# Kernel optimization log

Measured on AMD Instinct MI355X. Metric: run time of the kernel, lower is better.

## Reference

```python
import jax, jax.numpy as jnp
import numpy as np

EMBED_DIM = 1024
NUM_HEADS = 16
HEAD_DIM = EMBED_DIM // NUM_HEADS  # 64
SCALE = HEAD_DIM ** -0.5


def _rope_table(seq_len, dtype=jnp.float32):
    # inv_freq: [head_dim/2]
    inv_freq = 1.0 / (10000.0 ** (jnp.arange(0, HEAD_DIM, 2, dtype=dtype) / HEAD_DIM))
    t = jnp.arange(seq_len, dtype=dtype)
    freqs = t[:, None] * inv_freq[None, :]  # [S, hd/2]
    return jnp.sin(freqs), jnp.cos(freqs)


def _apply_rope(x, sin, cos):
    # x: [B, H, S, hd]; sin/cos: [S, hd/2]
    sin = sin[None, None]
    cos = cos[None, None]
    x_even = x[..., 0::2]
    x_odd = x[..., 1::2]
    new_even = x_even * cos - x_odd * sin
    new_odd = x_even * sin + x_odd * cos
    # interleave back: [..., hd/2, 2] -> [..., hd]
    return jnp.stack((new_even, new_odd), axis=-1).reshape(x.shape)


def setup_inputs() -> dict:
    key = jax.random.key(0)
    ks = jax.random.split(key, 9)
    B, S, D = 2, 2048, EMBED_DIM
    s = D ** -0.5
    return {
        "query": jax.random.normal(ks[0], (B, S, D), dtype=jnp.float32),
        "Wq": jax.random.normal(ks[1], (2 * D, D), dtype=jnp.float32) * s,
        "bq": jnp.zeros((2 * D,), dtype=jnp.float32),
        "Wk": jax.random.normal(ks[2], (D, D), dtype=jnp.float32) * s,
        "bk": jnp.zeros((D,), dtype=jnp.float32),
        "Wv": jax.random.normal(ks[3], (D, D), dtype=jnp.float32) * s,
        "bv": jnp.zeros((D,), dtype=jnp.float32),
        "Wo": jax.random.normal(ks[4], (D, D), dtype=jnp.float32) * s,
        "bo": jnp.zeros((D,), dtype=jnp.float32),
    }


def reference(query, Wq, bq, Wk, bk, Wv, bv, Wo, bo):
    B, S, D = query.shape
    H, hd = NUM_HEADS, HEAD_DIM

    # QKV projections (elementwise-gate variant: q_proj outputs 2*D)
    q_raw = (query @ Wq.T + bq).reshape(B, S, H, 2 * hd)
    q = q_raw[..., :hd].transpose(0, 2, 1, 3)          # [B,H,S,hd]
    gate = q_raw[..., hd:].transpose(0, 2, 1, 3)        # [B,H,S,hd]
    k = (query @ Wk.T + bk).reshape(B, S, H, hd).transpose(0, 2, 1, 3)
    v = (query @ Wv.T + bv).reshape(B, S, H, hd).transpose(0, 2, 1, 3)

    sin, cos = _rope_table(S)
    q = _apply_rope(q, sin, cos)
    k = _apply_rope(k, sin, cos)

    # scaled dot-product attention (no mask, non-causal, dropout=0)
    scores = jnp.einsum('bhqd,bhkd->bhqk', q, k) * SCALE
    probs = jax.nn.softmax(scores, axis=-1)
    attn = jnp.einsum('bhqk,bhkd->bhqd', probs, v)

    # sigmoid elementwise gate, then output projection
    attn = attn * jax.nn.sigmoid(gate)
    out = attn.transpose(0, 2, 1, 3).reshape(B, S, D)
    return out @ Wo.T + bo
```

## Files before the change

kernel.cpp:

```cpp
#include <hip/hip_runtime.h>
#include <math.h>

#define SEQ 2048
#define DIMD 1024
#define NH 16
#define HDIM 64

typedef _Float16 h8 __attribute__((ext_vector_type(8)));
typedef _Float16 h4 __attribute__((ext_vector_type(4)));
typedef __fp16 fp16x2 __attribute__((ext_vector_type(2)));
typedef float f32x4 __attribute__((ext_vector_type(4)));

typedef const __attribute__((address_space(1))) void* gas_t;
typedef __attribute__((address_space(3))) void* las_t;

__device__ __forceinline__ int SWE(int r, int c) {
  return ((r << 6) + c) ^ ((r & 7) << 3);
}

#define R0 16384
#define R1 (R0 + 1048576)
#define R2 (R1 + 524288)
#define R3 (R2 + 262144)
#define R4 (R3 + 262144)
#define R5 (R4 + 262144)

__global__ void prep_kernel(const float* __restrict__ query,
                            const float* __restrict__ Wq,
                            const float* __restrict__ Wk,
                            const float* __restrict__ Wv,
                            const float* __restrict__ Wo,
                            _Float16* __restrict__ Ah,
                            _Float16* __restrict__ Wqh,
                            _Float16* __restrict__ Wkh,
                            _Float16* __restrict__ Wvh,
                            _Float16* __restrict__ Woh,
                            float* __restrict__ sintab,
                            float* __restrict__ costab) {
  int i = blockIdx.x * 256 + threadIdx.x;
  if (i < R0) {
#pragma unroll
    for (int j = 0; j < 4; ++j) {
      int idx = i * 4 + j;
      int tp = idx >> 5;
      int fi = idx & 31;
      double inv = pow(10000.0, -(double)(2 * fi) / 64.0);
      double a = (double)tp * inv;
      sintab[idx] = (float)sin(a);
      costab[idx] = (float)cos(a);
    }
    return;
  }
  const float* src;
  _Float16* dst;
  int k;
  if (i < R1) {
    k = i - R0; src = query; dst = Ah;
  } else if (i < R2) {
    k = i - R1; src = Wq; dst = Wqh;
  } else if (i < R3) {
    k = i - R2; src = Wk; dst = Wkh;
  } else if (i < R4) {
    k = i - R3; src = Wv; dst = Wvh;
  } else if (i < R5) {
    k = i - R4; src = Wo; dst = Woh;
  } else {
    return;
  }
  float4 v = ((const float4*)src)[k];
  h4 H;
  H[0] = (_Float16)v.x;
  H[1] = (_Float16)v.y;
  H[2] = (_Float16)v.z;
  H[3] = (_Float16)v.w;
  ((h4*)dst)[k] = H;
}

__global__ __launch_bounds__(512) void qkv_kernel(
    const _Float16* __restrict__ Ah, const _Float16* __restrict__ Wqh,
    const _Float16* __restrict__ Wkh, const _Float16* __restrict__ Wvh,
    const float* __restrict__ bq, const float* __restrict__ bk,
    const float* __restrict__ bv, _Float16* __restrict__ qw,
    _Float16* __restrict__ sg, _Float16* __restrict__ kw,
    _Float16* __restrict__ vtw, const float* __restrict__ sintab,
    const float* __restrict__ costab) {
  __shared__ _Float16 Abuf[3][16384];
  __shared__ _Float16 Bbuf[3][8192];
  const int t = threadIdx.x;
  const int lane = t & 63;
  const int w = t >> 6;
  const int wm = w >> 1;
  const int wn = w & 1;
  const int fr = lane & 15;
  const int g = lane >> 4;
  const int m0 = blockIdx.y * 256;
  const int n0 = blockIdx.x * 128;
  const int region = (n0 < 2048) ? 0 : (n0 < 3072 ? 1 : 2);
  const _Float16* Wb = region == 0   ? Wqh + (size_t)n0 * DIMD
                       : region == 1 ? Wkh + (size_t)(n0 - 2048) * DIMD
                                     : Wvh + (size_t)(n0 - 3072) * DIMD;
  const float* bias = region == 0   ? bq + n0
                      : region == 1 ? bk + (n0 - 2048)
                                    : bv + (n0 - 3072);

  f32x4 acc[4][4];
#pragma unroll
  for (int i = 0; i < 4; ++i)
#pragma unroll
    for (int j = 0; j < 4; ++j) acc[i][j] = (f32x4){0.f, 0.f, 0.f, 0.f};

  const int rsub = t >> 3;
  const int csw = ((t & 7) ^ (rsub & 7)) << 3;
  const _Float16* gA = Ah + (size_t)(m0 + rsub) * DIMD + csw;
  const _Float16* gB = Wb + (size_t)rsub * DIMD + csw;

  auto stage = [&](int kt, int bi) {
#pragma unroll
    for (int i = 0; i < 4; ++i)
      __builtin_amdgcn_global_load_lds(
          (gas_t)(gA + (size_t)i * 64 * DIMD + kt * 64),
          (las_t)&Abuf[bi][i * 4096 + t * 8], 16, 0, 0);
#pragma unroll
    for (int i = 0; i < 2; ++i)
      __builtin_amdgcn_global_load_lds(
          (gas_t)(gB + (size_t)i * 64 * DIMD + kt * 64),
          (las_t)&Bbuf[bi][i * 4096 + t * 8], 16, 0, 0);
  };

  stage(0, 0);
  stage(1, 1);
  for (int kt = 0; kt < 16; ++kt) {
    const int cb = kt % 3;
    if (kt + 1 < 16) {
      asm volatile("s_waitcnt vmcnt(6)" ::: "memory");
    } else {
      asm volatile("s_waitcnt vmcnt(0)" ::: "memory");
    }
    if (kt + 2 < 16) stage(kt + 2, (kt + 2) % 3);
    __builtin_amdgcn_sched_barrier(0);
    __builtin_amdgcn_s_barrier();
    __builtin_amdgcn_sched_barrier(0);
#pragma unroll
    for (int kk = 0; kk < 2; ++kk) {
      h8 av[4], bv[4];
#pragma unroll
      for (int mi = 0; mi < 4; ++mi)
        av[mi] =
            *(const h8*)&Abuf[cb][SWE(wm * 64 + mi * 16 + fr, 8 * g + 32 * kk)];
#pragma unroll
      for (int ni = 0; ni < 4; ++ni)
        bv[ni] =
            *(const h8*)&Bbuf[cb][SWE(wn * 64 + ni * 16 + fr, 8 * g + 32 * kk)];
      __builtin_amdgcn_s_setprio(1);
#pragma unroll
      for (int mi = 0; mi < 4; ++mi)
#pragma unroll
        for (int ni = 0; ni < 4; ++ni)
          acc[mi][ni] = __builtin_amdgcn_mfma_f32_16x16x32_f16(
              av[mi], bv[ni], acc[mi][ni], 0, 0, 0);
      __builtin_amdgcn_s_setprio(0);
    }
    __builtin_amdgcn_s_barrier();
  }

#pragma unroll
  for (int mi = 0; mi < 4; ++mi)
#pragma unroll
    for (int ni = 0; ni < 4; ++ni) {
      const int cl = wn * 64 + ni * 16 + fr;
      const float bsv = bias[cl];
      if (region == 2) {
        const int vc = (n0 - 3072) + cl;
        const int h = vc >> 6, d = vc & 63;
        const int row0 = m0 + wm * 64 + mi * 16 + g * 4;
        const int b = row0 >> 11;
        const int s0 = row0 & (SEQ - 1);
        h4 vv;
#pragma unroll
        for (int r = 0; r < 4; ++r) vv[r] = (_Float16)(acc[mi][ni][r] + bsv);
        *(h4*)&vtw[((size_t)(b * NH + h) * HDIM + d) * SEQ + s0] = vv;
        continue;
      }
#pragma unroll
      for (int r = 0; r < 4; ++r) {
        const int row = m0 + wm * 64 + mi * 16 + g * 4 + r;
        float v = acc[mi][ni][r] + bsv;
        const int b = row >> 11;
        const int s = row & (SEQ - 1);
        if (region == 0) {
          const int h = n0 >> 7;
          const int d = cl & 63;
          if (wn == 0) {
            float vp = __shfl_xor(v, 1);
            const int pi = s * 32 + (d >> 1);
            float sn = sintab[pi], cs = costab[pi];
            float rv = (d & 1) ? (vp * sn + v * cs) : (v * cs - vp * sn);
            rv *= 0.125f;
            qw[((size_t)(b * NH + h) * SEQ + s) * HDIM + d] = (_Float16)rv;
          } else {
            float gv = 1.0f / (1.0f + __expf(-v));
            sg[((size_t)(b * SEQ + s)) * DIMD + h * HDIM + d] = (_Float16)gv;
          }
        } else {
          const int kc = (n0 - 2048) + cl;
          const int h = kc >> 6, d = kc & 63;
          float vp = __shfl_xor(v, 1);
          const int pi = s * 32 + (d >> 1);
          float sn = sintab[pi], cs = costab[pi];
          float rv = (d & 1) ? (vp * sn + v * cs) : (v * cs - vp * sn);
          kw[((size_t)(b * NH + h) * SEQ + s) * HDIM + d] = (_Float16)rv;
        }
      }
    }
}

__global__ __launch_bounds__(256) void ogemm_kernel(
    const _Float16* __restrict__ ag, const _Float16* __restrict__ Woh,
    const float* __restrict__ bias, float* __restrict__ out) {
  __shared__ _Float16 Abuf[8192];
  __shared__ _Float16 Bbuf[4096];
  const int t = threadIdx.x;
  const int lane = t & 63;
  const int w = t >> 6;
  const int wm = w & 1, wn = w >> 1;
  const int fr = lane & 15;
  const int g = lane >> 4;
  const int m0 = blockIdx.y * 128, n0 = blockIdx.x * 64;

  f32x4 acc[4][2];
#pragma unroll
  for (int i = 0; i < 4; ++i)
#pragma unroll
    for (int j = 0; j < 2; ++j) acc[i][j] = (f32x4){0.f, 0.f, 0.f, 0.f};

  const int rsub = t >> 3;
  const int csw = ((t & 7) ^ (rsub & 7)) << 3;
  const _Float16* gA = ag + (size_t)(m0 + rsub) * DIMD + csw;
  const _Float16* gB = Woh + (size_t)(n0 + rsub) * DIMD + csw;

  for (int kt = 0; kt < 16; ++kt) {
#pragma unroll
    for (int i = 0; i < 4; ++i)
      __builtin_amdgcn_global_load_lds(
          (gas_t)(gA + (size_t)i * 32 * DIMD + kt * 64),
          (las_t)&Abuf[i * 2048 + t * 8], 16, 0, 0);
#pragma unroll
    for (int i = 0; i < 2; ++i)
      __builtin_amdgcn_global_load_lds(
          (gas_t)(gB + (size_t)i * 32 * DIMD + kt * 64),
          (las_t)&Bbuf[i * 2048 + t * 8], 16, 0, 0);
    __syncthreads();
#pragma unroll
    for (int s = 0; s < 2; ++s) {
      h8 av[4], bv[2];
#pragma unroll
      for (int mi = 0; mi < 4; ++mi)
        av[mi] = *(const h8*)&Abuf[SWE(wm * 64 + mi * 16 + fr, 8 * g + 32 * s)];
#pragma unroll
      for (int ni = 0; ni < 2; ++ni)
        bv[ni] = *(const h8*)&Bbuf[SWE(wn * 32 + ni * 16 + fr, 8 * g + 32 * s)];
      __builtin_amdgcn_s_setprio(1);
#pragma unroll
      for (int mi = 0; mi < 4; ++mi)
#pragma unroll
        for (int ni = 0; ni < 2; ++ni)
          acc[mi][ni] = __builtin_amdgcn_mfma_f32_16x16x32_f16(
              av[mi], bv[ni], acc[mi][ni], 0, 0, 0);
      __builtin_amdgcn_s_setprio(0);
    }
    __syncthreads();
  }

#pragma unroll
  for (int mi = 0; mi < 4; ++mi)
#pragma unroll
    for (int ni = 0; ni < 2; ++ni) {
      const int col = n0 + wn * 32 + ni * 16 + fr;
      const float bsv = bias[col];
#pragma unroll
      for (int r = 0; r < 4; ++r) {
        const int row = m0 + wm * 64 + mi * 16 + g * 4 + r;
        out[(size_t)row * DIMD + col] = acc[mi][ni][r] + bsv;
      }
    }
}

__global__ __launch_bounds__(256) void flash_kernel(
    const _Float16* __restrict__ qh, const _Float16* __restrict__ kh,
    const _Float16* __restrict__ vt, const _Float16* __restrict__ sg,
    _Float16* __restrict__ ag) {
  __shared__ _Float16 K_lds[4096];
  __shared__ _Float16 Vt_lds[4096];
  const int t = threadIdx.x;
  const int lane = t & 63;
  const int w = t >> 6;
  const int fr = lane & 15;
  const int g = lane >> 4;
  const int flat = blockIdx.x;
  const int swz = (flat & 7) * 128 + (flat >> 3);
  const int bh = swz >> 5;
  const int q0 = (swz & 31) * 64;
  const size_t kvbase = (size_t)bh * (SEQ * HDIM);

  h8 qb[2];
  {
    const _Float16* qp = qh + kvbase + (size_t)(q0 + 16 * w + fr) * HDIM + 8 * g;
    qb[0] = *(const h8*)(qp);
    qb[1] = *(const h8*)(qp + 32);
  }

  f32x4 oacc[4];
  float m_i = -1e30f, l_i = 0.f;
#pragma unroll
  for (int df = 0; df < 4; ++df) oacc[df] = (f32x4){0.f, 0.f, 0.f, 0.f};

  const int srow = t >> 2;
  const int scb = (t & 3) * 16;
  const int vbase = ((scb >> 4) >> 1) * 32 + ((scb >> 4) & 1) * 4;
  const _Float16* kp = kh + kvbase;
  const _Float16* vp = vt + kvbase + (size_t)srow * SEQ;

  h8 k0v = *(const h8*)(kp + (size_t)srow * HDIM + scb);
  h8 k1v = *(const h8*)(kp + (size_t)srow * HDIM + scb + 8);
  h8 v0v = *(const h8*)(vp + scb);
  h8 v1v = *(const h8*)(vp + scb + 8);

  for (int j0 = 0; j0 < SEQ; j0 += 64) {
    __syncthreads();
    *(h8*)&K_lds[SWE(srow, scb)] = k0v;
    *(h8*)&K_lds[SWE(srow, scb + 8)] = k1v;
    {
      h4 a0 = __builtin_shufflevector(v0v, v0v, 0, 1, 2, 3);
      h4 a1 = __builtin_shufflevector(v0v, v0v, 4, 5, 6, 7);
      h4 b0 = __builtin_shufflevector(v1v, v1v, 0, 1, 2, 3);
      h4 b1 = __builtin_shufflevector(v1v, v1v, 4, 5, 6, 7);
      *(h4*)&Vt_lds[SWE(srow, vbase)] = a0;
      *(h4*)&Vt_lds[SWE(srow, vbase + 8)] = a1;
      *(h4*)&Vt_lds[SWE(srow, vbase + 16)] = b0;
      *(h4*)&Vt_lds[SWE(srow, vbase + 24)] = b1;
    }
    if (j0 + 64 < SEQ) {
      k0v = *(const h8*)(kp + (size_t)(j0 + 64 + srow) * HDIM + scb);
      k1v = *(const h8*)(kp + (size_t)(j0 + 64 + srow) * HDIM + scb + 8);
      v0v = *(const h8*)(vp + j0 + 64 + scb);
      v1v = *(const h8*)(vp + j0 + 64 + scb + 8);
    }
    __syncthreads();

    f32x4 sacc[4];
#pragma unroll
    for (int nf = 0; nf < 4; ++nf) sacc[nf] = (f32x4){0.f, 0.f, 0.f, 0.f};

    __builtin_amdgcn_s_setprio(1);
#pragma unroll
    for (int nf = 0; nf < 4; ++nf) {
      h8 ka0 = *(const h8*)&K_lds[SWE(16 * nf + fr, 8 * g)];
      h8 ka1 = *(const h8*)&K_lds[SWE(16 * nf + fr, 32 + 8 * g)];
      sacc[nf] =
          __builtin_amdgcn_mfma_f32_16x16x32_f16(ka0, qb[0], sacc[nf], 0, 0, 0);
      sacc[nf] =
          __builtin_amdgcn_mfma_f32_16x16x32_f16(ka1, qb[1], sacc[nf], 0, 0, 0);
    }
    __builtin_amdgcn_s_setprio(0);

    float m0 = fmaxf(fmaxf(sacc[0][0], sacc[0][1]), sacc[0][2]);
    float m1 = fmaxf(fmaxf(sacc[0][3], sacc[1][0]), sacc[1][1]);
    float m2 = fmaxf(fmaxf(sacc[1][2], sacc[1][3]), sacc[2][0]);
    float m3 = fmaxf(fmaxf(sacc[2][1], sacc[2][2]), sacc[2][3]);
    float m4 = fmaxf(fmaxf(sacc[3][0], sacc[3][1]), sacc[3][2]);
    float mx =
        fmaxf(fmaxf(fmaxf(fmaxf(m0, m1), m2), fmaxf(m3, m4)), sacc[3][3]);
    mx = fmaxf(mx, __shfl_xor(mx, 16));
    mx = fmaxf(mx, __shfl_xor(mx, 32));
    const int allskip = __all(mx <= m_i + 8.0f);
    const float mn = allskip ? m_i : fmaxf(m_i, mx);
    float p[4][4];
    float rs = 0.f;
#pragma unroll
    for (int nf = 0; nf < 4; ++nf)
#pragma unroll
      for (int r = 0; r < 4; ++r) {
        p[nf][r] = __expf(sacc[nf][r] - mn);
        rs += p[nf][r];
      }
    rs += __shfl_xor(rs, 16);
    rs += __shfl_xor(rs, 32);
    if (allskip) {
      l_i += rs;
    } else {
      float f = __expf(m_i - mn);
      l_i = l_i * f + rs;
      m_i = mn;
      f32x4 fv = (f32x4){f, f, f, f};
#pragma unroll
      for (int df = 0; df < 4; ++df) oacc[df] *= fv;
    }
    h8 pb[2];
#pragma unroll
    for (int m2i = 0; m2i < 2; ++m2i) {
      union {
        h8 v;
        fp16x2 h[4];
      } u;
      u.h[0] = __builtin_amdgcn_cvt_pkrtz(p[2 * m2i][0], p[2 * m2i][1]);
      u.h[1] = __builtin_amdgcn_cvt_pkrtz(p[2 * m2i][2], p[2 * m2i][3]);
      u.h[2] = __builtin_amdgcn_cvt_pkrtz(p[2 * m2i + 1][0], p[2 * m2i + 1][1]);
      u.h[3] = __builtin_amdgcn_cvt_pkrtz(p[2 * m2i + 1][2], p[2 * m2i + 1][3]);
      pb[m2i] = u.v;
    }

    __builtin_amdgcn_s_setprio(1);
#pragma unroll
    for (int df = 0; df < 4; ++df) {
#pragma unroll
      for (int m2i = 0; m2i < 2; ++m2i) {
        h8 va = *(const h8*)&Vt_lds[SWE(16 * df + fr, m2i * 32 + 8 * g)];
        oacc[df] =
            __builtin_amdgcn_mfma_f32_16x16x32_f16(va, pb[m2i], oacc[df], 0, 0, 0);
      }
    }
    __builtin_amdgcn_s_setprio(0);
  }

  const int b = bh >> 4, h = bh & 15;
  const int qrow = q0 + 16 * w + fr;
  const float inv = 1.0f / l_i;
  const size_t obase = ((size_t)(b * SEQ + qrow)) * DIMD + h * HDIM;
#pragma unroll
  for (int df = 0; df < 4; ++df) {
    const int d0 = 16 * df + 4 * g;
    h4 gt = *(const h4*)&sg[obase + d0];
    h4 ov;
#pragma unroll
    for (int r = 0; r < 4; ++r)
      ov[r] = (_Float16)(oacc[df][r] * inv * (float)gt[r]);
    *(h4*)&ag[obase + d0] = ov;
  }
}

extern "C" void kernel_launch(void* const* d_in, const int* in_sizes, int n_in,
                              void* d_out, int out_size, void* d_ws,
                              size_t ws_size, hipStream_t stream) {
  const float* query = (const float*)d_in[0];
  const float* Wq = (const float*)d_in[1];
  const float* bq = (const float*)d_in[2];
  const float* Wk = (const float*)d_in[3];
  const float* bk = (const float*)d_in[4];
  const float* Wv = (const float*)d_in[5];
  const float* bv = (const float*)d_in[6];
  const float* Wo = (const float*)d_in[7];
  const float* bo = (const float*)d_in[8];
  float* out = (float*)d_out;

  float* fws = (float*)d_ws;
  float* sintab = fws;
  float* costab = fws + 65536;
  _Float16* Ah = (_Float16*)(fws + 131072);
  _Float16* Wqh = Ah + 4194304;
  _Float16* Wkh = Wqh + 2097152;
  _Float16* Wvh = Wkh + 1048576;
  _Float16* Woh = Wvh + 1048576;
  _Float16* qw = Woh + 1048576;
  _Float16* kw = qw + 4194304;
  _Float16* vtw = kw + 4194304;
  _Float16* sg = vtw + 4194304;
  _Float16* ag = Ah;

  prep_kernel<<<9280, 256, 0, stream>>>(query, Wq, Wk, Wv, Wo, Ah, Wqh, Wkh,
                                        Wvh, Woh, sintab, costab);

  qkv_kernel<<<dim3(32, 16), 512, 0, stream>>>(Ah, Wqh, Wkh, Wvh, bq, bk, bv,
                                               qw, sg, kw, vtw, sintab, costab);

  flash_kernel<<<1024, 256, 0, stream>>>(qw, kw, vtw, sg, ag);

  ogemm_kernel<<<dim3(16, 32), 256, 0, stream>>>(ag, Woh, bo, out);
}
```

Measured before the change: 164.8 us.

## Enlarge QKV GEMM tile to 256x256 with quarter-staged double buffering

The QKV projection GEMM moves from 256x128 to 256x256 block tiles, with 8 waves laid out 2x4 and each wave owning a 128x64 sub-tile. The triple-buffered LDS pipeline becomes a double buffer whose next-k loads are issued in four quarter-stages interleaved with four compute sub-steps, with extra barriers. This aims to raise arithmetic intensity and cut redundant global loads of A. The trade-offs are a grid halved to 256 blocks (close to one wave of CUs), higher register pressure from 128 accumulator floats per thread, and more barriers per k-step.

```diff
diff --git a/kernel.cpp b/kernel.cpp
--- a/kernel.cpp
+++ b/kernel.cpp
@@ -76,7 +76,7 @@
   ((h4*)dst)[k] = H;
 }
 
-__global__ __launch_bounds__(512) void qkv_kernel(
+__global__ __launch_bounds__(512, 2) void qkv_kernel(
     const _Float16* __restrict__ Ah, const _Float16* __restrict__ Wqh,
     const _Float16* __restrict__ Wkh, const _Float16* __restrict__ Wvh,
     const float* __restrict__ bq, const float* __restrict__ bk,
@@ -84,95 +84,114 @@
     _Float16* __restrict__ sg, _Float16* __restrict__ kw,
     _Float16* __restrict__ vtw, const float* __restrict__ sintab,
     const float* __restrict__ costab) {
-  __shared__ _Float16 Abuf[3][16384];
-  __shared__ _Float16 Bbuf[3][8192];
+  __shared__ _Float16 Abuf[2][16384];
+  __shared__ _Float16 Bbuf[2][16384];
   const int t = threadIdx.x;
   const int lane = t & 63;
   const int w = t >> 6;
-  const int wm = w >> 1;
-  const int wn = w & 1;
+  const int wm = w >> 2;
+  const int wn = w & 3;
   const int fr = lane & 15;
   const int g = lane >> 4;
   const int m0 = blockIdx.y * 256;
-  const int n0 = blockIdx.x * 128;
+  const int n0 = blockIdx.x * 256;
   const int region = (n0 < 2048) ? 0 : (n0 < 3072 ? 1 : 2);
   const _Float16* Wb = region == 0   ? Wqh + (size_t)n0 * DIMD
                        : region == 1 ? Wkh + (size_t)(n0 - 2048) * DIMD
                                      : Wvh + (size_t)(n0 - 3072) * DIMD;
-  const float* bias = region == 0   ? bq + n0
-                      : region == 1 ? bk + (n0 - 2048)
-                                    : bv + (n0 - 3072);
-
-  f32x4 acc[4][4];
-#pragma unroll
-  for (int i = 0; i < 4; ++i)
+
+  f32x4 acc[8][4];
+#pragma unroll
+  for (int i = 0; i < 8; ++i)
 #pragma unroll
     for (int j = 0; j < 4; ++j) acc[i][j] = (f32x4){0.f, 0.f, 0.f, 0.f};
 
-  const int rsub = t >> 3;
-  const int csw = ((t & 7) ^ (rsub & 7)) << 3;
-  const _Float16* gA = Ah + (size_t)(m0 + rsub) * DIMD + csw;
-  const _Float16* gB = Wb + (size_t)rsub * DIMD + csw;
-
-  auto stage = [&](int kt, int bi) {
-#pragma unroll
-    for (int i = 0; i < 4; ++i)
-      __builtin_amdgcn_global_load_lds(
-          (gas_t)(gA + (size_t)i * 64 * DIMD + kt * 64),
-          (las_t)&Abuf[bi][i * 4096 + t * 8], 16, 0, 0);
-#pragma unroll
-    for (int i = 0; i < 2; ++i)
-      __builtin_amdgcn_global_load_lds(
-          (gas_t)(gB + (size_t)i * 64 * DIMD + kt * 64),
-          (las_t)&Bbuf[bi][i * 4096 + t * 8], 16, 0, 0);
+  const int csw = ((t & 7) ^ ((t >> 3) & 7)) << 3;
+  const _Float16* gA = Ah + (size_t)(m0 + (t >> 3)) * DIMD + csw;
+  const _Float16* gB = Wb + (size_t)(t >> 3) * DIMD + csw;
+
+  auto stage_half = [&](int kt, int hf, int sl) {
+    const int r0 = (hf & 1) * 128;
+    if (hf < 2) {
+#pragma unroll
+      for (int i = 0; i < 2; ++i)
+        __builtin_amdgcn_global_load_lds(
+            (gas_t)(gA + (size_t)(r0 + i * 64) * DIMD + kt * 64),
+            (las_t)&Abuf[sl][(hf & 1) * 8192 + (i * 512 + t) * 8], 16, 0, 0);
+    } else {
+#pragma unroll
+      for (int i = 0; i < 2; ++i)
+        __builtin_amdgcn_global_load_lds(
+            (gas_t)(gB + (size_t)(r0 + i * 64) * DIMD + kt * 64),
+            (las_t)&Bbuf[sl][(hf & 1) * 8192 + (i * 512 + t) * 8], 16, 0, 0);
+    }
   };
 
-  stage(0, 0);
-  stage(1, 1);
+#pragma unroll
+  for (int hf = 0; hf < 4; ++hf) stage_half(0, hf, 0);
+
   for (int kt = 0; kt < 16; ++kt) {
-    const int cb = kt % 3;
-    if (kt + 1 < 16) {
-      asm volatile("s_waitcnt vmcnt(6)" ::: "memory");
-    } else {
-      asm volatile("s_waitcnt vmcnt(0)" ::: "memory");
-    }
-    if (kt + 2 < 16) stage(kt + 2, (kt + 2) % 3);
-    __builtin_amdgcn_sched_barrier(0);
-    __builtin_amdgcn_s_barrier();
-    __builtin_amdgcn_sched_barrier(0);
-#pragma unroll
-    for (int kk = 0; kk < 2; ++kk) {
-      h8 av[4], bv[4];
+    const int sl = kt & 1;
+#pragma unroll
+    for (int q = 0; q < 4; ++q) {
+      const int mh = q >> 1, nh = q & 1;
+      if (kt + 1 < 16) stage_half(kt + 1, q, sl ^ 1);
+      if (q == 0) {
+        if (kt + 1 < 16)
+          asm volatile("s_waitcnt vmcnt(2)" ::: "memory");
+        else
+          asm volatile("s_waitcnt vmcnt(0)" ::: "memory");
+        __builtin_amdgcn_sched_barrier(0);
+        __builtin_amdgcn_s_barrier();
+      }
+      h8 av[4][2], bv[2][2];
 #pragma unroll
       for (int mi = 0; mi < 4; ++mi)
-        av[mi] =
-            *(const h8*)&Abuf[cb][SWE(wm * 64 + mi * 16 + fr, 8 * g + 32 * kk)];
-#pragma unroll
-      for (int ni = 0; ni < 4; ++ni)
-        bv[ni] =
-            *(const h8*)&Bbuf[cb][SWE(wn * 64 + ni * 16 + fr, 8 * g + 32 * kk)];
+#pragma unroll
+        for (int kk = 0; kk < 2; ++kk)
+          av[mi][kk] = *(const h8*)&Abuf[sl][wm * 8192 +
+                                            SWE(mh * 64 + mi * 16 + fr,
+                                                8 * g + 32 * kk)];
+#pragma unroll
+      for (int ni = 0; ni < 2; ++ni)
+#pragma unroll
+        for (int kk = 0; kk < 2; ++kk)
+          bv[ni][kk] = *(const h8*)&Bbuf[sl][(wn >> 1) * 8192 +
+                                             SWE((wn & 1) * 64 + nh * 32 +
+                                                     ni * 16 + fr,
+                                                 8 * g + 32 * kk)];
+      if (q != 0) __builtin_amdgcn_s_barrier();
+      asm volatile("s_waitcnt lgkmcnt(0)" ::: "memory");
+      __builtin_amdgcn_sched_barrier(0);
       __builtin_amdgcn_s_setprio(1);
 #pragma unroll
-      for (int mi = 0; mi < 4; ++mi)
-#pragma unroll
-        for (int ni = 0; ni < 4; ++ni)
-          acc[mi][ni] = __builtin_amdgcn_mfma_f32_16x16x32_f16(
-              av[mi], bv[ni], acc[mi][ni], 0, 0, 0);
+      for (int kk = 0; kk < 2; ++kk)
+#pragma unroll
+        for (int mi = 0; mi < 4; ++mi)
+#pragma unroll
+          for (int ni = 0; ni < 2; ++ni)
+            acc[mh * 4 + mi][nh * 2 + ni] =
+                __builtin_amdgcn_mfma_f32_16x16x32_f16(
+                    av[mi][kk], bv[ni][kk], acc[mh * 4 + mi][nh * 2 + ni], 0,
+                    0, 0);
       __builtin_amdgcn_s_setprio(0);
-    }
-    __builtin_amdgcn_s_barrier();
-  }
-
-#pragma unroll
-  for (int mi = 0; mi < 4; ++mi)
+      __builtin_amdgcn_s_barrier();
+    }
+  }
+
+#pragma unroll
+  for (int mi = 0; mi < 8; ++mi)
 #pragma unroll
     for (int ni = 0; ni < 4; ++ni) {
-      const int cl = wn * 64 + ni * 16 + fr;
-      const float bsv = bias[cl];
+      const int colg = n0 + wn * 64 + (ni >> 1) * 32 + (ni & 1) * 16 + fr;
+      const float bsv = region == 0   ? bq[colg]
+                        : region == 1 ? bk[colg - 2048]
+                                      : bv[colg - 3072];
+      const int row0 =
+          m0 + wm * 128 + (mi >> 2) * 64 + (mi & 3) * 16 + g * 4;
       if (region == 2) {
-        const int vc = (n0 - 3072) + cl;
+        const int vc = colg - 3072;
         const int h = vc >> 6, d = vc & 63;
-        const int row0 = m0 + wm * 64 + mi * 16 + g * 4;
         const int b = row0 >> 11;
         const int s0 = row0 & (SEQ - 1);
         h4 vv;
@@ -183,14 +202,14 @@
       }
 #pragma unroll
       for (int r = 0; r < 4; ++r) {
-        const int row = m0 + wm * 64 + mi * 16 + g * 4 + r;
+        const int row = row0 + r;
         float v = acc[mi][ni][r] + bsv;
         const int b = row >> 11;
         const int s = row & (SEQ - 1);
         if (region == 0) {
-          const int h = n0 >> 7;
-          const int d = cl & 63;
-          if (wn == 0) {
+          const int h = colg >> 7;
+          const int d = colg & 63;
+          if (((colg >> 6) & 1) == 0) {
             float vp = __shfl_xor(v, 1);
             const int pi = s * 32 + (d >> 1);
             float sn = sintab[pi], cs = costab[pi];
@@ -202,7 +221,7 @@
             sg[((size_t)(b * SEQ + s)) * DIMD + h * HDIM + d] = (_Float16)gv;
           }
         } else {
-          const int kc = (n0 - 2048) + cl;
+          const int kc = colg - 2048;
           const int h = kc >> 6, d = kc & 63;
           float vp = __shfl_xor(v, 1);
           const int pi = s * 32 + (d >> 1);
@@ -469,7 +488,7 @@
   prep_kernel<<<9280, 256, 0, stream>>>(query, Wq, Wk, Wv, Wo, Ah, Wqh, Wkh,
                                         Wvh, Woh, sintab, costab);
 
-  qkv_kernel<<<dim3(32, 16), 512, 0, stream>>>(Ah, Wqh, Wkh, Wvh, bq, bk, bv,
+  qkv_kernel<<<dim3(16, 16), 512, 0, stream>>>(Ah, Wqh, Wkh, Wvh, bq, bk, bv,
                                                qw, sg, kw, vtw, sintab, costab);
 
   flash_kernel<<<1024, 256, 0, stream>>>(qw, kw, vtw, sg, ag);
```

Result: slower. 176.9 us (+7.3%).
